# Optimization experiments

Measured on AMD Instinct MI355X. Metric: run time of the kernel, lower is better.

## Reference

```python
import jax, jax.numpy as jnp
import numpy as np

N = 50000      # nodes
E = 800000     # edges (avg degree 16)
IN, HID, OUT = 128, 128, 64


def setup_inputs() -> dict:
    key = jax.random.key(0)
    ks = jax.random.split(key, 8)
    x = jax.random.normal(ks[0], (N, IN), dtype=jnp.float32)
    edge_index = jax.random.randint(ks[1], (2, E), 0, N, dtype=jnp.int64)
    s1 = 1.0 / np.sqrt(IN)
    s2 = 1.0 / np.sqrt(HID)
    # SAGEConv params: lin_l acts on aggregated neighbors (has bias), lin_r on root
    W1l = jax.random.uniform(ks[2], (IN, HID), jnp.float32, -s1, s1)
    W1r = jax.random.uniform(ks[3], (IN, HID), jnp.float32, -s1, s1)
    b1 = jax.random.uniform(ks[4], (HID,), jnp.float32, -s1, s1)
    W2l = jax.random.uniform(ks[5], (HID, OUT), jnp.float32, -s2, s2)
    W2r = jax.random.uniform(ks[6], (HID, OUT), jnp.float32, -s2, s2)
    b2 = jax.random.uniform(ks[7], (OUT,), jnp.float32, -s2, s2)
    return {"x": x, "edge_index": edge_index, "W1l": W1l, "W1r": W1r,
            "b1": b1, "W2l": W2l, "W2r": W2r, "b2": b2}


def reference(x, edge_index, W1l, W1r, b1, W2l, W2r, b2):
    src = edge_index[0]
    dst = edge_index[1]
    n = x.shape[0]
    deg = jax.ops.segment_sum(jnp.ones(src.shape, x.dtype), dst, num_segments=n)
    inv_deg = (1.0 / jnp.maximum(deg, 1.0))[:, None]  # [N,1], avoid div-by-zero

    def mean_agg(h):
        # gather neighbor feats, scatter-sum to destination, normalize by in-degree
        return jax.ops.segment_sum(h[src], dst, num_segments=n) * inv_deg

    # SAGEConv layer 1: lin_l(mean_j x_j) + lin_r(x_i), then ReLU (dropout off in eval)
    h = mean_agg(x) @ W1l + x @ W1r + b1
    h = jax.nn.relu(h)
    # SAGEConv layer 2
    out = mean_agg(h) @ W2l + h @ W2r + b2
    return out
```

## Files before the change

kernel.cpp:

```cpp
#include <hip/hip_runtime.h>
#include <hip/hip_bf16.h>


typedef __attribute__((ext_vector_type(8))) short bf16x8;
typedef __attribute__((ext_vector_type(4))) float f32x4;

__device__ __forceinline__ ushort f2b(float f) {
    uint u = __float_as_uint(f);
    return (ushort)((u + 0x7fffu + ((u >> 16) & 1u)) >> 16);
}
__device__ __forceinline__ float b2f(ushort h) { return __uint_as_float(((uint)h) << 16); }
__device__ __forceinline__ float blo(uint u) { return __uint_as_float(u << 16); }
__device__ __forceinline__ float bhi(uint u) { return __uint_as_float(u & 0xffff0000u); }

__global__ void count_deg_k(const int* __restrict__ dstv, int* __restrict__ cnt, int E) {
    int e = blockIdx.x * blockDim.x + threadIdx.x;
    if (e < E) atomicAdd(&cnt[dstv[e]], 1);
}

__global__ __launch_bounds__(256) void blocksum_k(const int* __restrict__ cnt,
                                                  int* __restrict__ bsum, int n) {
    __shared__ int red[4];
    int b = blockIdx.x, t = threadIdx.x;
    int base = b * 1024 + t * 4;
    int s = 0;
    #pragma unroll
    for (int i = 0; i < 4; ++i) { int idx = base + i; if (idx < n) s += cnt[idx]; }
    #pragma unroll
    for (int off = 32; off > 0; off >>= 1) s += __shfl_down(s, off);
    if ((t & 63) == 0) red[t >> 6] = s;
    __syncthreads();
    if (t == 0) bsum[b] = red[0] + red[1] + red[2] + red[3];
}

__global__ __launch_bounds__(256) void bscan_k(int* __restrict__ bsum, int nb) {
    __shared__ int sd[256];
    int t = threadIdx.x;
    int v = (t < nb) ? bsum[t] : 0;
    sd[t] = v;
    __syncthreads();
    for (int off = 1; off < 256; off <<= 1) {
        int u = (t >= off) ? sd[t - off] : 0;
        __syncthreads();
        sd[t] += u;
        __syncthreads();
    }
    if (t < nb) bsum[t] = sd[t] - v;
}

__global__ __launch_bounds__(256) void scanout_k(const int* __restrict__ cnt,
                                                 const int* __restrict__ bbase,
                                                 int* __restrict__ rowptr,
                                                 int* __restrict__ pos,
                                                 float* __restrict__ inv_deg,
                                                 int n, int E) {
    __shared__ int sums[256];
    int b = blockIdx.x, t = threadIdx.x;
    int base = b * 1024 + t * 4;
    int v[4];
    int s = 0;
    #pragma unroll
    for (int i = 0; i < 4; ++i) {
        int idx = base + i;
        v[i] = (idx < n) ? cnt[idx] : 0;
        s += v[i];
    }
    sums[t] = s;
    __syncthreads();
    for (int off = 1; off < 256; off <<= 1) {
        int u = (t >= off) ? sums[t - off] : 0;
        __syncthreads();
        sums[t] += u;
        __syncthreads();
    }
    int pre = sums[t] - s + bbase[b];
    #pragma unroll
    for (int i = 0; i < 4; ++i) {
        int idx = base + i;
        if (idx < n) {
            rowptr[idx] = pre;
            pos[idx] = pre;
            inv_deg[idx] = 1.0f / (float)max(v[i], 1);
            pre += v[i];
        }
    }
    if (b == 0 && t == 0) rowptr[n] = E;
}

__global__ void bucketbase_k(const int* __restrict__ rowptr, int* __restrict__ bucketPos,
                             int nbuckets) {
    int b = blockIdx.x * blockDim.x + threadIdx.x;
    if (b < nbuckets) bucketPos[b] = rowptr[b * 256];
}

__global__ __launch_bounds__(256) void bucket_k(const int* __restrict__ srcv,
                                                const int* __restrict__ dstv,
                                                int* __restrict__ bucketPos,
                                                uint2* __restrict__ ebuf, int E) {
    __shared__ int hist[256], rbase[256];
    int t = threadIdx.x;
    int e0 = blockIdx.x * 2048;
    hist[t] = 0;
    __syncthreads();
    int d[8], s[8];
    #pragma unroll
    for (int i = 0; i < 8; ++i) {
        int e = e0 + t + 256 * i;
        if (e < E) {
            d[i] = dstv[e]; s[i] = srcv[e];
            atomicAdd(&hist[d[i] >> 8], 1);
        } else d[i] = -1;
    }
    __syncthreads();
    if (hist[t] > 0) rbase[t] = atomicAdd(&bucketPos[t], hist[t]);
    __syncthreads();
    hist[t] = 0;
    __syncthreads();
    #pragma unroll
    for (int i = 0; i < 8; ++i) {
        if (d[i] >= 0) {
            int b = d[i] >> 8;
            int off = atomicAdd(&hist[b], 1);
            ebuf[rbase[b] + off] = make_uint2((uint)d[i], (uint)s[i]);
        }
    }
}

__global__ void fill2_k(const uint2* __restrict__ ebuf, int* __restrict__ pos,
                        int* __restrict__ csr, int E) {
    int e = blockIdx.x * blockDim.x + threadIdx.x;
    if (e < E) {
        uint2 v = ebuf[e];
        int p = atomicAdd(&pos[v.x], 1);
        csr[p] = (int)v.y;
    }
}

__global__ void castx_k(const float* __restrict__ x, ushort* __restrict__ xb, int total4) {
    int i = blockIdx.x * blockDim.x + threadIdx.x;
    if (i < total4) {
        float4 v = reinterpret_cast<const float4*>(x)[i];
        ushort4 r;
        r.x = f2b(v.x); r.y = f2b(v.y); r.z = f2b(v.z); r.w = f2b(v.w);
        reinterpret_cast<ushort4*>(xb)[i] = r;
    }
}

__global__ void prepw_k(const float* __restrict__ W1l, const float* __restrict__ W1r,
                        const float* __restrict__ W2l, const float* __restrict__ W2r,
                        ushort* __restrict__ w1lt, ushort* __restrict__ w1rt,
                        ushort* __restrict__ w2lt, ushort* __restrict__ w2rt) {
    int i = blockIdx.x * blockDim.x + threadIdx.x;
    if (i < 16384) {
        int nn = i >> 7, k = i & 127;
        w1lt[i] = f2b(W1l[k * 128 + nn]);
    } else if (i < 32768) {
        int j = i - 16384, nn = j >> 7, k = j & 127;
        w1rt[j] = f2b(W1r[k * 128 + nn]);
    } else if (i < 40960) {
        int j = i - 32768, nn = j >> 7, k = j & 127;
        w2lt[j] = f2b(W2l[k * 64 + nn]);
    } else if (i < 49152) {
        int j = i - 40960, nn = j >> 7, k = j & 127;
        w2rt[j] = f2b(W2r[k * 64 + nn]);
    }
}

template<int F>
__global__ __launch_bounds__(256) void aggb_k(const ushort* __restrict__ feat,
                                              const int* __restrict__ rowptr,
                                              const int* __restrict__ csr,
                                              const float* __restrict__ invd,
                                              ushort* __restrict__ out, int n) {
    int tid = blockIdx.x * 256 + threadIdx.x;
    int node = tid >> 5;
    int sl = threadIdx.x & 31;
    if (node >= n) return;
    int s = rowptr[node], e = rowptr[node + 1];
    float sc = invd[node];
    if (F == 128) {
        float a0 = 0, a1 = 0, a2 = 0, a3 = 0;
        int p = s;
        for (; p + 2 <= e; p += 2) {
            int u0 = csr[p], u1 = csr[p + 1];
            uint2 v0 = *reinterpret_cast<const uint2*>(&feat[(size_t)u0 * 128 + sl * 4]);
            uint2 v1 = *reinterpret_cast<const uint2*>(&feat[(size_t)u1 * 128 + sl * 4]);
            a0 += blo(v0.x); a1 += bhi(v0.x); a2 += blo(v0.y); a3 += bhi(v0.y);
            a0 += blo(v1.x); a1 += bhi(v1.x); a2 += blo(v1.y); a3 += bhi(v1.y);
        }
        if (p < e) {
            uint2 v0 = *reinterpret_cast<const uint2*>(&feat[(size_t)csr[p] * 128 + sl * 4]);
            a0 += blo(v0.x); a1 += bhi(v0.x); a2 += blo(v0.y); a3 += bhi(v0.y);
        }
        ushort4 r;
        r.x = f2b(a0 * sc); r.y = f2b(a1 * sc); r.z = f2b(a2 * sc); r.w = f2b(a3 * sc);
        *reinterpret_cast<ushort4*>(&out[(size_t)node * 128 + sl * 4]) = r;
    } else {
        float a0 = 0, a1 = 0;
        int p = s;
        for (; p + 2 <= e; p += 2) {
            int u0 = csr[p], u1 = csr[p + 1];
            uint v0 = *reinterpret_cast<const uint*>(&feat[(size_t)u0 * 64 + sl * 2]);
            uint v1 = *reinterpret_cast<const uint*>(&feat[(size_t)u1 * 64 + sl * 2]);
            a0 += blo(v0) + blo(v1); a1 += bhi(v0) + bhi(v1);
        }
        if (p < e) {
            uint v0 = *reinterpret_cast<const uint*>(&feat[(size_t)csr[p] * 64 + sl * 2]);
            a0 += blo(v0); a1 += bhi(v0);
        }
        ushort2 r;
        r.x = f2b(a0 * sc); r.y = f2b(a1 * sc);
        *reinterpret_cast<ushort2*>(&out[(size_t)node * 64 + sl * 2]) = r;
    }
}

template<int NC, int NSRC, bool RELU, bool OUT_BF16, bool HAS_BIAS, bool HAS_ADD>
__global__ __launch_bounds__(256) void mgemm_k(const ushort* __restrict__ A0,
                                               const ushort* __restrict__ B0,
                                               const ushort* __restrict__ A1,
                                               const ushort* __restrict__ B1,
                                               const ushort* __restrict__ addm,
                                               const float* __restrict__ bias,
                                               void* __restrict__ Cout, int n) {
    constexpr int AST = 136;
    __shared__ ushort At[64 * AST];
    __shared__ ushort Bt[NC * AST];
    int t = threadIdx.x;
    int brow = blockIdx.x * 64;
    int w = t >> 6, l = t & 63, lrow = l & 15, lk = l >> 4;

    f32x4 acc[NC / 16];
    #pragma unroll
    for (int g = 0; g < NC / 16; ++g) acc[g] = (f32x4){0.f, 0.f, 0.f, 0.f};

    #pragma unroll
    for (int src = 0; src < NSRC; ++src) {
        const ushort* A = src ? A1 : A0;
        const ushort* B = src ? B1 : B0;
        __syncthreads();
        #pragma unroll
        for (int i = 0; i < 4; ++i) {
            int c = t + 256 * i, r = c >> 4, k16 = c & 15;
            int grow = brow + r;
            uint4 v = make_uint4(0, 0, 0, 0);
            if (grow < n) v = *reinterpret_cast<const uint4*>(&A[(size_t)grow * 128 + k16 * 8]);
            *reinterpret_cast<uint4*>(&At[r * AST + k16 * 8]) = v;
        }
        #pragma unroll
        for (int i = 0; i < NC / 16; ++i) {
            int c = t + 256 * i, r = c >> 4, k16 = c & 15;
            *reinterpret_cast<uint4*>(&Bt[r * AST + k16 * 8]) =
                *reinterpret_cast<const uint4*>(&B[(size_t)r * 128 + k16 * 8]);
        }
        __syncthreads();
        #pragma unroll
        for (int ks = 0; ks < 4; ++ks) {
            bf16x8 a = *reinterpret_cast<const bf16x8*>(&At[(w * 16 + lrow) * AST + ks * 32 + lk * 8]);
            #pragma unroll
            for (int g = 0; g < NC / 16; ++g) {
                bf16x8 b = *reinterpret_cast<const bf16x8*>(&Bt[(g * 16 + lrow) * AST + ks * 32 + lk * 8]);
                acc[g] = __builtin_amdgcn_mfma_f32_16x16x32_bf16(a, b, acc[g], 0, 0, 0);
            }
        }
    }

    int orow = brow + w * 16 + lk * 4;
    #pragma unroll
    for (int g = 0; g < NC / 16; ++g) {
        int gcol = g * 16 + lrow;
        float bv = HAS_BIAS ? bias[gcol] : 0.f;
        #pragma unroll
        for (int r = 0; r < 4; ++r) {
            int grow = orow + r;
            if (grow >= n) continue;
            float o = acc[g][r] + bv;
            if (HAS_ADD) o += b2f(addm[(size_t)grow * NC + gcol]);
            if (RELU) o = fmaxf(o, 0.f);
            if (OUT_BF16) ((ushort*)Cout)[(size_t)grow * NC + gcol] = f2b(o);
            else          ((float*)Cout)[(size_t)grow * NC + gcol] = o;
        }
    }
}

extern "C" void kernel_launch(void* const* d_in, const int* in_sizes, int n_in,
                              void* d_out, int out_size, void* d_ws, size_t ws_size,
                              hipStream_t stream) {
    const float* x   = (const float*)d_in[0];
    const int*   edge= (const int*)d_in[1];
    const float* W1l = (const float*)d_in[2];
    const float* W1r = (const float*)d_in[3];
    const float* b1  = (const float*)d_in[4];
    const float* W2l = (const float*)d_in[5];
    const float* W2r = (const float*)d_in[6];
    const float* b2  = (const float*)d_in[7];
    float* out = (float*)d_out;

    const int N = in_sizes[0] / 128;
    const int E = in_sizes[1] / 2;
    const int* srcv = edge;
    const int* dstv = edge + E;

    char* p = (char*)d_ws;
    auto alloc = [&](size_t bytes) {
        char* q = p;
        p += ((bytes + 255) & ~(size_t)255);
        return q;
    };
    int*    cnt    = (int*)alloc((size_t)N * 4);
    int*    rowptr = (int*)alloc((size_t)(N + 1) * 4);
    int*    pos    = (int*)alloc((size_t)N * 4);
    int*    csr    = (int*)alloc((size_t)E * 4);
    float*  invd   = (float*)alloc((size_t)N * 4);
    int*    bsum   = (int*)alloc((size_t)256 * 4);
    int*    bktpos = (int*)alloc((size_t)256 * 4);
    uint2*  ebuf   = (uint2*)alloc((size_t)E * 8);
    ushort* xb     = (ushort*)alloc((size_t)N * 128 * 2);
    ushort* tbuf   = (ushort*)alloc((size_t)N * 128 * 2);
    ushort* h      = (ushort*)alloc((size_t)N * 128 * 2);
    ushort* hl     = (ushort*)alloc((size_t)N * 64 * 2);
    ushort* t2     = (ushort*)alloc((size_t)N * 64 * 2);
    ushort* w1lt   = (ushort*)alloc((size_t)16384 * 2);
    ushort* w1rt   = (ushort*)alloc((size_t)16384 * 2);
    ushort* w2lt   = (ushort*)alloc((size_t)8192 * 2);
    ushort* w2rt   = (ushort*)alloc((size_t)8192 * 2);

    int nb = (N + 1023) / 1024;
    int nbuckets = (N + 255) / 256;

    castx_k<<<(N * 32 + 255) / 256, 256, 0, stream>>>(x, xb, N * 32);
    prepw_k<<<192, 256, 0, stream>>>(W1l, W1r, W2l, W2r, w1lt, w1rt, w2lt, w2rt);

    hipMemsetAsync(cnt, 0, (size_t)N * 4, stream);
    count_deg_k<<<(E + 255) / 256, 256, 0, stream>>>(dstv, cnt, E);
    blocksum_k<<<nb, 256, 0, stream>>>(cnt, bsum, N);
    bscan_k<<<1, 256, 0, stream>>>(bsum, nb);
    scanout_k<<<nb, 256, 0, stream>>>(cnt, bsum, rowptr, pos, invd, N, E);
    bucketbase_k<<<1, 256, 0, stream>>>(rowptr, bktpos, nbuckets);
    bucket_k<<<(E + 2047) / 2048, 256, 0, stream>>>(srcv, dstv, bktpos, ebuf, E);
    fill2_k<<<(E + 255) / 256, 256, 0, stream>>>(ebuf, pos, csr, E);

    int gb = (N + 63) / 64;
    int ag = (N + 7) / 8;

    aggb_k<128><<<ag, 256, 0, stream>>>(xb, rowptr, csr, invd, tbuf, N);
    mgemm_k<128, 2, true, true, true, false><<<gb, 256, 0, stream>>>(
        xb, w1rt, tbuf, w1lt, nullptr, b1, h, N);
    mgemm_k<64, 1, false, true, false, false><<<gb, 256, 0, stream>>>(
        h, w2lt, nullptr, nullptr, nullptr, nullptr, hl, N);
    aggb_k<64><<<ag, 256, 0, stream>>>(hl, rowptr, csr, invd, t2, N);
    mgemm_k<64, 1, false, false, true, true><<<gb, 256, 0, stream>>>(
        h, w2rt, nullptr, nullptr, t2, b2, out, N);
}
```

Measured before the change: 271.6 us.

## Fuse neighbor mean aggregation into layer GEMM kernels via shared memory

Folds the layer-1 gather/mean aggregation into the first GEMM kernel, writing aggregated rows into shared memory instead of a global buffer. It also folds the layer-2 aggregation of the projected features into the final GEMM epilogue. This removes two kernel launches and the global round-trips of the intermediate aggregate buffers. In exchange, the gather now runs inside 64-row GEMM blocks with fewer resident waves and a larger unroll-by-4. That may reduce the latency hiding available for the random-access gathers.

```diff
diff --git a/kernel.cpp b/kernel.cpp
--- a/kernel.cpp
+++ b/kernel.cpp
@@ -166,118 +166,253 @@
     }
 }
 
-template<int F>
-__global__ __launch_bounds__(256) void aggb_k(const ushort* __restrict__ feat,
-                                              const int* __restrict__ rowptr,
-                                              const int* __restrict__ csr,
-                                              const float* __restrict__ invd,
-                                              ushort* __restrict__ out, int n) {
-    int tid = blockIdx.x * 256 + threadIdx.x;
-    int node = tid >> 5;
-    int sl = threadIdx.x & 31;
-    if (node >= n) return;
-    int s = rowptr[node], e = rowptr[node + 1];
-    float sc = invd[node];
-    if (F == 128) {
-        float a0 = 0, a1 = 0, a2 = 0, a3 = 0;
-        int p = s;
-        for (; p + 2 <= e; p += 2) {
-            int u0 = csr[p], u1 = csr[p + 1];
-            uint2 v0 = *reinterpret_cast<const uint2*>(&feat[(size_t)u0 * 128 + sl * 4]);
-            uint2 v1 = *reinterpret_cast<const uint2*>(&feat[(size_t)u1 * 128 + sl * 4]);
-            a0 += blo(v0.x); a1 += bhi(v0.x); a2 += blo(v0.y); a3 += bhi(v0.y);
-            a0 += blo(v1.x); a1 += bhi(v1.x); a2 += blo(v1.y); a3 += bhi(v1.y);
-        }
-        if (p < e) {
-            uint2 v0 = *reinterpret_cast<const uint2*>(&feat[(size_t)csr[p] * 128 + sl * 4]);
-            a0 += blo(v0.x); a1 += bhi(v0.x); a2 += blo(v0.y); a3 += bhi(v0.y);
-        }
-        ushort4 r;
-        r.x = f2b(a0 * sc); r.y = f2b(a1 * sc); r.z = f2b(a2 * sc); r.w = f2b(a3 * sc);
-        *reinterpret_cast<ushort4*>(&out[(size_t)node * 128 + sl * 4]) = r;
-    } else {
-        float a0 = 0, a1 = 0;
-        int p = s;
-        for (; p + 2 <= e; p += 2) {
-            int u0 = csr[p], u1 = csr[p + 1];
-            uint v0 = *reinterpret_cast<const uint*>(&feat[(size_t)u0 * 64 + sl * 2]);
-            uint v1 = *reinterpret_cast<const uint*>(&feat[(size_t)u1 * 64 + sl * 2]);
-            a0 += blo(v0) + blo(v1); a1 += bhi(v0) + bhi(v1);
-        }
-        if (p < e) {
-            uint v0 = *reinterpret_cast<const uint*>(&feat[(size_t)csr[p] * 64 + sl * 2]);
-            a0 += blo(v0); a1 += bhi(v0);
-        }
-        ushort2 r;
-        r.x = f2b(a0 * sc); r.y = f2b(a1 * sc);
-        *reinterpret_cast<ushort2*>(&out[(size_t)node * 64 + sl * 2]) = r;
-    }
-}
-
-template<int NC, int NSRC, bool RELU, bool OUT_BF16, bool HAS_BIAS, bool HAS_ADD>
-__global__ __launch_bounds__(256) void mgemm_k(const ushort* __restrict__ A0,
-                                               const ushort* __restrict__ B0,
-                                               const ushort* __restrict__ A1,
-                                               const ushort* __restrict__ B1,
-                                               const ushort* __restrict__ addm,
-                                               const float* __restrict__ bias,
-                                               void* __restrict__ Cout, int n) {
+__global__ __launch_bounds__(256) void mg1_k(const ushort* __restrict__ xb,
+                                             const ushort* __restrict__ w1rt,
+                                             const ushort* __restrict__ w1lt,
+                                             const int* __restrict__ rowptr,
+                                             const int* __restrict__ csr,
+                                             const float* __restrict__ invd,
+                                             const float* __restrict__ b1,
+                                             ushort* __restrict__ h, int n) {
     constexpr int AST = 136;
     __shared__ ushort At[64 * AST];
-    __shared__ ushort Bt[NC * AST];
+    __shared__ ushort Bt[128 * AST];
     int t = threadIdx.x;
     int brow = blockIdx.x * 64;
     int w = t >> 6, l = t & 63, lrow = l & 15, lk = l >> 4;
 
-    f32x4 acc[NC / 16];
-    #pragma unroll
-    for (int g = 0; g < NC / 16; ++g) acc[g] = (f32x4){0.f, 0.f, 0.f, 0.f};
-
-    #pragma unroll
-    for (int src = 0; src < NSRC; ++src) {
-        const ushort* A = src ? A1 : A0;
-        const ushort* B = src ? B1 : B0;
-        __syncthreads();
-        #pragma unroll
-        for (int i = 0; i < 4; ++i) {
-            int c = t + 256 * i, r = c >> 4, k16 = c & 15;
-            int grow = brow + r;
-            uint4 v = make_uint4(0, 0, 0, 0);
-            if (grow < n) v = *reinterpret_cast<const uint4*>(&A[(size_t)grow * 128 + k16 * 8]);
-            *reinterpret_cast<uint4*>(&At[r * AST + k16 * 8]) = v;
-        }
-        #pragma unroll
-        for (int i = 0; i < NC / 16; ++i) {
-            int c = t + 256 * i, r = c >> 4, k16 = c & 15;
-            *reinterpret_cast<uint4*>(&Bt[r * AST + k16 * 8]) =
-                *reinterpret_cast<const uint4*>(&B[(size_t)r * 128 + k16 * 8]);
-        }
-        __syncthreads();
-        #pragma unroll
-        for (int ks = 0; ks < 4; ++ks) {
-            bf16x8 a = *reinterpret_cast<const bf16x8*>(&At[(w * 16 + lrow) * AST + ks * 32 + lk * 8]);
-            #pragma unroll
-            for (int g = 0; g < NC / 16; ++g) {
-                bf16x8 b = *reinterpret_cast<const bf16x8*>(&Bt[(g * 16 + lrow) * AST + ks * 32 + lk * 8]);
-                acc[g] = __builtin_amdgcn_mfma_f32_16x16x32_bf16(a, b, acc[g], 0, 0, 0);
+    f32x4 acc[8];
+    #pragma unroll
+    for (int g = 0; g < 8; ++g) acc[g] = (f32x4){0.f, 0.f, 0.f, 0.f};
+
+    #pragma unroll
+    for (int i = 0; i < 4; ++i) {
+        int c = t + 256 * i, r = c >> 4, k16 = c & 15;
+        int grow = brow + r;
+        uint4 v = make_uint4(0, 0, 0, 0);
+        if (grow < n) v = *reinterpret_cast<const uint4*>(&xb[(size_t)grow * 128 + k16 * 8]);
+        *reinterpret_cast<uint4*>(&At[r * AST + k16 * 8]) = v;
+    }
+    #pragma unroll
+    for (int i = 0; i < 8; ++i) {
+        int c = t + 256 * i, r = c >> 4, k16 = c & 15;
+        *reinterpret_cast<uint4*>(&Bt[r * AST + k16 * 8]) =
+            *reinterpret_cast<const uint4*>(&w1rt[(size_t)r * 128 + k16 * 8]);
+    }
+    __syncthreads();
+    #pragma unroll
+    for (int ks = 0; ks < 4; ++ks) {
+        bf16x8 a = *reinterpret_cast<const bf16x8*>(&At[(w * 16 + lrow) * AST + ks * 32 + lk * 8]);
+        #pragma unroll
+        for (int g = 0; g < 8; ++g) {
+            bf16x8 b = *reinterpret_cast<const bf16x8*>(&Bt[(g * 16 + lrow) * AST + ks * 32 + lk * 8]);
+            acc[g] = __builtin_amdgcn_mfma_f32_16x16x32_bf16(a, b, acc[g], 0, 0, 0);
+        }
+    }
+    __syncthreads();
+
+    int hw = t >> 5, sl = t & 31;
+    for (int i = 0; i < 8; ++i) {
+        int lr = i * 8 + hw;
+        int node = brow + lr;
+        float a0 = 0, a1 = 0, a2 = 0, a3 = 0;
+        if (node < n) {
+            int s = rowptr[node], e = rowptr[node + 1];
+            float sc = invd[node];
+            int p = s;
+            for (; p + 4 <= e; p += 4) {
+                int u0 = csr[p], u1 = csr[p + 1], u2 = csr[p + 2], u3 = csr[p + 3];
+                uint2 v0 = *reinterpret_cast<const uint2*>(&xb[(size_t)u0 * 128 + sl * 4]);
+                uint2 v1 = *reinterpret_cast<const uint2*>(&xb[(size_t)u1 * 128 + sl * 4]);
+                uint2 v2 = *reinterpret_cast<const uint2*>(&xb[(size_t)u2 * 128 + sl * 4]);
+                uint2 v3 = *reinterpret_cast<const uint2*>(&xb[(size_t)u3 * 128 + sl * 4]);
+                a0 += blo(v0.x) + blo(v1.x) + blo(v2.x) + blo(v3.x);
+                a1 += bhi(v0.x) + bhi(v1.x) + bhi(v2.x) + bhi(v3.x);
+                a2 += blo(v0.y) + blo(v1.y) + blo(v2.y) + blo(v3.y);
+                a3 += bhi(v0.y) + bhi(v1.y) + bhi(v2.y) + bhi(v3.y);
             }
+            for (; p < e; ++p) {
+                uint2 v0 = *reinterpret_cast<const uint2*>(&xb[(size_t)csr[p] * 128 + sl * 4]);
+                a0 += blo(v0.x); a1 += bhi(v0.x); a2 += blo(v0.y); a3 += bhi(v0.y);
+            }
+            a0 *= sc; a1 *= sc; a2 *= sc; a3 *= sc;
+        }
+        ushort4 r4;
+        r4.x = f2b(a0); r4.y = f2b(a1); r4.z = f2b(a2); r4.w = f2b(a3);
+        *reinterpret_cast<ushort4*>(&At[lr * AST + sl * 4]) = r4;
+    }
+    #pragma unroll
+    for (int i = 0; i < 8; ++i) {
+        int c = t + 256 * i, r = c >> 4, k16 = c & 15;
+        *reinterpret_cast<uint4*>(&Bt[r * AST + k16 * 8]) =
+            *reinterpret_cast<const uint4*>(&w1lt[(size_t)r * 128 + k16 * 8]);
+    }
+    __syncthreads();
+    #pragma unroll
+    for (int ks = 0; ks < 4; ++ks) {
+        bf16x8 a = *reinterpret_cast<const bf16x8*>(&At[(w * 16 + lrow) * AST + ks * 32 + lk * 8]);
+        #pragma unroll
+        for (int g = 0; g < 8; ++g) {
+            bf16x8 b = *reinterpret_cast<const bf16x8*>(&Bt[(g * 16 + lrow) * AST + ks * 32 + lk * 8]);
+            acc[g] = __builtin_amdgcn_mfma_f32_16x16x32_bf16(a, b, acc[g], 0, 0, 0);
         }
     }
 
     int orow = brow + w * 16 + lk * 4;
     #pragma unroll
-    for (int g = 0; g < NC / 16; ++g) {
+    for (int g = 0; g < 8; ++g) {
         int gcol = g * 16 + lrow;
-        float bv = HAS_BIAS ? bias[gcol] : 0.f;
+        float bv = b1[gcol];
         #pragma unroll
         for (int r = 0; r < 4; ++r) {
             int grow = orow + r;
             if (grow >= n) continue;
-            float o = acc[g][r] + bv;
-            if (HAS_ADD) o += b2f(addm[(size_t)grow * NC + gcol]);
-            if (RELU) o = fmaxf(o, 0.f);
-            if (OUT_BF16) ((ushort*)Cout)[(size_t)grow * NC + gcol] = f2b(o);
-            else          ((float*)Cout)[(size_t)grow * NC + gcol] = o;
+            float o = fmaxf(acc[g][r] + bv, 0.f);
+            h[(size_t)grow * 128 + gcol] = f2b(o);
+        }
+    }
+}
+
+__global__ __launch_bounds__(256) void mg2_k(const ushort* __restrict__ A,
+                                             const ushort* __restrict__ B,
+                                             ushort* __restrict__ C, int n) {
+    constexpr int AST = 136;
+    __shared__ ushort At[64 * AST];
+    __shared__ ushort Bt[64 * AST];
+    int t = threadIdx.x;
+    int brow = blockIdx.x * 64;
+    int w = t >> 6, l = t & 63, lrow = l & 15, lk = l >> 4;
+
+    f32x4 acc[4];
+    #pragma unroll
+    for (int g = 0; g < 4; ++g) acc[g] = (f32x4){0.f, 0.f, 0.f, 0.f};
+
+    #pragma unroll
+    for (int i = 0; i < 4; ++i) {
+        int c = t + 256 * i, r = c >> 4, k16 = c & 15;
+        int grow = brow + r;
+        uint4 v = make_uint4(0, 0, 0, 0);
+        if (grow < n) v = *reinterpret_cast<const uint4*>(&A[(size_t)grow * 128 + k16 * 8]);
+        *reinterpret_cast<uint4*>(&At[r * AST + k16 * 8]) = v;
+    }
+    #pragma unroll
+    for (int i = 0; i < 4; ++i) {
+        int c = t + 256 * i, r = c >> 4, k16 = c & 15;
+        *reinterpret_cast<uint4*>(&Bt[r * AST + k16 * 8]) =
+            *reinterpret_cast<const uint4*>(&B[(size_t)r * 128 + k16 * 8]);
+    }
+    __syncthreads();
+    #pragma unroll
+    for (int ks = 0; ks < 4; ++ks) {
+        bf16x8 a = *reinterpret_cast<const bf16x8*>(&At[(w * 16 + lrow) * AST + ks * 32 + lk * 8]);
+        #pragma unroll
+        for (int g = 0; g < 4; ++g) {
+            bf16x8 b = *reinterpret_cast<const bf16x8*>(&Bt[(g * 16 + lrow) * AST + ks * 32 + lk * 8]);
+            acc[g] = __builtin_amdgcn_mfma_f32_16x16x32_bf16(a, b, acc[g], 0, 0, 0);
+        }
+    }
+
+    int orow = brow + w * 16 + lk * 4;
+    #pragma unroll
+    for (int g = 0; g < 4; ++g) {
+        int gcol = g * 16 + lrow;
+        #pragma unroll
+        for (int r = 0; r < 4; ++r) {
+            int grow = orow + r;
+            if (grow >= n) continue;
+            C[(size_t)grow * 64 + gcol] = f2b(acc[g][r]);
+        }
+    }
+}
+
+__global__ __launch_bounds__(256) void mg3_k(const ushort* __restrict__ h,
+                                             const ushort* __restrict__ w2rt,
+                                             const ushort* __restrict__ hl,
+                                             const int* __restrict__ rowptr,
+                                             const int* __restrict__ csr,
+                                             const float* __restrict__ invd,
+                                             const float* __restrict__ b2,
+                                             float* __restrict__ out, int n) {
+    constexpr int AST = 136;
+    constexpr int TST = 66;
+    __shared__ ushort At[64 * AST];
+    __shared__ ushort Bt[64 * AST];
+    __shared__ ushort Tadd[64 * TST];
+    int t = threadIdx.x;
+    int brow = blockIdx.x * 64;
+    int w = t >> 6, l = t & 63, lrow = l & 15, lk = l >> 4;
+
+    f32x4 acc[4];
+    #pragma unroll
+    for (int g = 0; g < 4; ++g) acc[g] = (f32x4){0.f, 0.f, 0.f, 0.f};
+
+    #pragma unroll
+    for (int i = 0; i < 4; ++i) {
+        int c = t + 256 * i, r = c >> 4, k16 = c & 15;
+        int grow = brow + r;
+        uint4 v = make_uint4(0, 0, 0, 0);
+        if (grow < n) v = *reinterpret_cast<const uint4*>(&h[(size_t)grow * 128 + k16 * 8]);
+        *reinterpret_cast<uint4*>(&At[r * AST + k16 * 8]) = v;
+    }
+    #pragma unroll
+    for (int i = 0; i < 4; ++i) {
+        int c = t + 256 * i, r = c >> 4, k16 = c & 15;
+        *reinterpret_cast<uint4*>(&Bt[r * AST + k16 * 8]) =
+            *reinterpret_cast<const uint4*>(&w2rt[(size_t)r * 128 + k16 * 8]);
+    }
+    __syncthreads();
+    #pragma unroll
+    for (int ks = 0; ks < 4; ++ks) {
+        bf16x8 a = *reinterpret_cast<const bf16x8*>(&At[(w * 16 + lrow) * AST + ks * 32 + lk * 8]);
+        #pragma unroll
+        for (int g = 0; g < 4; ++g) {
+            bf16x8 b = *reinterpret_cast<const bf16x8*>(&Bt[(g * 16 + lrow) * AST + ks * 32 + lk * 8]);
+            acc[g] = __builtin_amdgcn_mfma_f32_16x16x32_bf16(a, b, acc[g], 0, 0, 0);
+        }
+    }
+
+    int hw = t >> 5, sl = t & 31;
+    for (int i = 0; i < 8; ++i) {
+        int lr = i * 8 + hw;
+        int node = brow + lr;
+        float a0 = 0, a1 = 0;
+        if (node < n) {
+            int s = rowptr[node], e = rowptr[node + 1];
+            float sc = invd[node];
+            int p = s;
+            for (; p + 4 <= e; p += 4) {
+                int u0 = csr[p], u1 = csr[p + 1], u2 = csr[p + 2], u3 = csr[p + 3];
+                uint v0 = *reinterpret_cast<const uint*>(&hl[(size_t)u0 * 64 + sl * 2]);
+                uint v1 = *reinterpret_cast<const uint*>(&hl[(size_t)u1 * 64 + sl * 2]);
+                uint v2 = *reinterpret_cast<const uint*>(&hl[(size_t)u2 * 64 + sl * 2]);
+                uint v3 = *reinterpret_cast<const uint*>(&hl[(size_t)u3 * 64 + sl * 2]);
+                a0 += blo(v0) + blo(v1) + blo(v2) + blo(v3);
+                a1 += bhi(v0) + bhi(v1) + bhi(v2) + bhi(v3);
+            }
+            for (; p < e; ++p) {
+                uint v0 = *reinterpret_cast<const uint*>(&hl[(size_t)csr[p] * 64 + sl * 2]);
+                a0 += blo(v0); a1 += bhi(v0);
+            }
+            a0 *= sc; a1 *= sc;
+        }
+        ushort2 r2;
+        r2.x = f2b(a0); r2.y = f2b(a1);
+        *reinterpret_cast<ushort2*>(&Tadd[lr * TST + sl * 2]) = r2;
+    }
+    __syncthreads();
+
+    int orow = brow + w * 16 + lk * 4;
+    #pragma unroll
+    for (int g = 0; g < 4; ++g) {
+        int gcol = g * 16 + lrow;
+        float bv = b2[gcol];
+        #pragma unroll
+        for (int r = 0; r < 4; ++r) {
+            int grow = orow + r;
+            if (grow >= n) continue;
+            int lrr = w * 16 + lk * 4 + r;
+            float o = acc[g][r] + bv + b2f(Tadd[lrr * TST + gcol]);
+            out[(size_t)grow * 64 + gcol] = o;
         }
     }
 }
@@ -315,10 +450,8 @@
     int*    bktpos = (int*)alloc((size_t)256 * 4);
     uint2*  ebuf   = (uint2*)alloc((size_t)E * 8);
     ushort* xb     = (ushort*)alloc((size_t)N * 128 * 2);
-    ushort* tbuf   = (ushort*)alloc((size_t)N * 128 * 2);
     ushort* h      = (ushort*)alloc((size_t)N * 128 * 2);
     ushort* hl     = (ushort*)alloc((size_t)N * 64 * 2);
-    ushort* t2     = (ushort*)alloc((size_t)N * 64 * 2);
     ushort* w1lt   = (ushort*)alloc((size_t)16384 * 2);
     ushort* w1rt   = (ushort*)alloc((size_t)16384 * 2);
     ushort* w2lt   = (ushort*)alloc((size_t)8192 * 2);
@@ -340,14 +473,7 @@
     fill2_k<<<(E + 255) / 256, 256, 0, stream>>>(ebuf, pos, csr, E);
 
     int gb = (N + 63) / 64;
-    int ag = (N + 7) / 8;
-
-    aggb_k<128><<<ag, 256, 0, stream>>>(xb, rowptr, csr, invd, tbuf, N);
-    mgemm_k<128, 2, true, true, true, false><<<gb, 256, 0, stream>>>(
-        xb, w1rt, tbuf, w1lt, nullptr, b1, h, N);
-    mgemm_k<64, 1, false, true, false, false><<<gb, 256, 0, stream>>>(
-        h, w2lt, nullptr, nullptr, nullptr, nullptr, hl, N);
-    aggb_k<64><<<ag, 256, 0, stream>>>(hl, rowptr, csr, invd, t2, N);
-    mgemm_k<64, 1, false, false, true, true><<<gb, 256, 0, stream>>>(
-        h, w2rt, nullptr, nullptr, t2, b2, out, N);
-}
+    mg1_k<<<gb, 256, 0, stream>>>(xb, w1rt, w1lt, rowptr, csr, invd, b1, h, N);
+    mg2_k<<<gb, 256, 0, stream>>>(h, w2lt, hl, N);
+    mg3_k<<<gb, 256, 0, stream>>>(h, w2rt, hl, rowptr, csr, invd, b2, out, N);
+}
```

New measurement: 340.3 us. 1.25x slower.
